# Optimization experiments

Measured on AMD Instinct MI355X. Metric: run time of the kernel, lower is better.

## Reference

```python
import jax, jax.numpy as jnp
import numpy as np

N = 4_194_304  # total points
C = 2          # classes: 0=ground, 1=plant
B = 8          # number of point clouds in the batch
SIGMA_L = 0.1
SIGMA_R = 0.4
CLAMP_FACTOR = 2.0
MIN_VAL = 0.1
FOCAL_GAMMA = 2.0
FOCAL_ALPHA = 1.0
LOSS_WEIGHT = 1.0


def setup_inputs() -> dict:
    key = jax.random.key(0)
    k1, k2, k3 = jax.random.split(key, 3)
    pred = jax.random.normal(k1, (N, C), dtype=jnp.float32)
    coord = jax.random.normal(k2, (N, 3), dtype=jnp.float32)
    segment = jax.random.randint(k3, (N,), 0, C, dtype=jnp.int32)
    # pointcept-style cumulative offsets: equal-sized clouds, offset[-1] == N
    offset = (jnp.arange(1, B + 1, dtype=jnp.int32) * (N // B))
    return {"pred": pred, "coord": coord, "segment": segment, "offset": offset}


def _gauss_weights(z, segment, batch):
    # per-cloud z_ground_max (fallback: z.min) and z_plant_min (fallback: z.max)
    neg_inf = jnp.array(-jnp.inf, z.dtype)
    pos_inf = jnp.array(jnp.inf, z.dtype)
    gmax = jax.ops.segment_max(jnp.where(segment == 0, z, neg_inf), batch, num_segments=B)
    pmin = jax.ops.segment_min(jnp.where(segment == 1, z, pos_inf), batch, num_segments=B)
    has_g = jax.ops.segment_sum((segment == 0).astype(z.dtype), batch, num_segments=B) > 0
    has_p = jax.ops.segment_sum((segment == 1).astype(z.dtype), batch, num_segments=B) > 0
    zmin = jax.ops.segment_min(z, batch, num_segments=B)
    zmax = jax.ops.segment_max(z, batch, num_segments=B)
    g = jnp.where(has_g, gmax, zmin)
    p = jnp.where(has_p, pmin, zmax)
    mu_b = g + (p - g) * 0.5  # (B,)
    mu = mu_b[batch]          # (N,)
    d = z - mu
    w_left = jnp.exp(-(d * d) / (2.0 * SIGMA_L * SIGMA_L))
    w_right = jnp.exp(-(d * d) / (2.0 * SIGMA_R * SIGMA_R))
    w_right = jnp.where(d > CLAMP_FACTOR * SIGMA_R, jnp.array(MIN_VAL, z.dtype), w_right)
    return jnp.where(z <= mu, w_left, w_right)


def reference(pred, coord, segment, offset):
    n = pred.shape[0]
    # offset2batch: per-point batch id from cumulative offsets
    batch = jnp.searchsorted(offset, jnp.arange(n, dtype=offset.dtype), side='right')
    # cross entropy (reduction='none')
    logp = jax.nn.log_softmax(pred, axis=1)              # (N, C)
    logp_t = jnp.take_along_axis(logp, segment[:, None], axis=1)[:, 0]  # (N,)
    seg_loss = (-logp_t) * LOSS_WEIGHT
    # focal reweighting (computed under no_grad in the original)
    p_t = jax.lax.stop_gradient(jnp.exp(logp_t))
    focal_weight = FOCAL_ALPHA * (1.0 - p_t) ** FOCAL_GAMMA
    seg_loss = seg_loss * focal_weight
    # asymmetric gaussian z-weighting, segment-conditioned per cloud
    weights = _gauss_weights(coord[:, 2], segment, batch)
    return jnp.mean(seg_loss * weights)
```

## Files before the change

### kernel.cpp

```cpp
#include <hip/hip_runtime.h>
#include <math.h>

#define THREADS 1024
#define NBLOCKS 256
#define UNROLL  8

__device__ __forceinline__ unsigned enc_f(float f) {
    unsigned b = __float_as_uint(f);
    return (b & 0x80000000u) ? ~b : (b | 0x80000000u);
}
__device__ __forceinline__ float dec_f(unsigned u) {
    unsigned b = (u & 0x80000000u) ? (u ^ 0x80000000u) : ~u;
    return __uint_as_float(b);
}
#define ENC_NEG_INF 0x007FFFFFu
#define ENC_POS_INF 0xFF800000u
__device__ __forceinline__ unsigned ident_w(int w) {
    return (w < 8 || w >= 24) ? ENC_NEG_INF : ENC_POS_INF;
}

#define SLOT(base, blk) ((base) + 64 + (blk) * 32)

#define CNT_B(ii, bdst) do { bdst = 0; \
    _Pragma("unroll") for (int j_ = 0; j_ < 8; ++j_) bdst += ((ii) >= roff[j_]); } while (0)

#define FLUSH_LDS(bb, g_, p_, mn_, mx_) do { \
    atomicMax(&s_stats[      (bb)], enc_f(g_));  \
    atomicMin(&s_stats[ 8  + (bb)], enc_f(p_));  \
    atomicMin(&s_stats[16  + (bb)], enc_f(mn_)); \
    atomicMax(&s_stats[24  + (bb)], enc_f(mx_)); } while (0)

__global__ __launch_bounds__(THREADS) void k_stats(
        const float* __restrict__ coord, const int* __restrict__ segment,
        const int* __restrict__ offset, unsigned* __restrict__ ws, int n, int nb) {
    __shared__ unsigned s_stats[32];
    const int tid = threadIdx.x;
    if (tid < 32) s_stats[tid] = ident_w(tid);
    if (blockIdx.x == 0 && tid == THREADS - 1) {
        *(double*)(ws + 32) = 0.0;
        ws[34] = 0u;
    }
    int roff[8];
    #pragma unroll
    for (int j = 0; j < 8; ++j) roff[j] = (j < nb) ? offset[j] : 0x7FFFFFFF;
    __syncthreads();

    const int chunk = (n + (int)gridDim.x - 1) / (int)gridDim.x;
    const int start = blockIdx.x * chunk;
    const int end   = min(n, start + chunk);

    float lg = -INFINITY, lp = INFINITY, lmn = INFINITY, lmx = -INFINITY;

    if (start < end) {
        int ba = 0, bb = 0;
        #pragma unroll
        for (int j = 0; j < 8; ++j) { ba += (start >= roff[j]); bb += ((end - 1) >= roff[j]); }
        if (ba == bb) {
            int i = start + tid;
            for (; i + (UNROLL - 1) * THREADS < end; i += UNROLL * THREADS) {
                float z[UNROLL]; int s[UNROLL];
                #pragma unroll
                for (int k = 0; k < UNROLL; ++k) z[k] = coord[3 * (i + k * THREADS) + 2];
                #pragma unroll
                for (int k = 0; k < UNROLL; ++k) s[k] = segment[i + k * THREADS];
                #pragma unroll
                for (int k = 0; k < UNROLL; ++k) {
                    lmn = fminf(lmn, z[k]);
                    lmx = fmaxf(lmx, z[k]);
                    lg  = fmaxf(lg, (s[k] == 0) ? z[k] : -INFINITY);
                    lp  = fminf(lp, (s[k] != 0) ? z[k] : INFINITY);
                }
            }
            for (; i < end; i += THREADS) {
                float z = coord[3 * i + 2]; int s = segment[i];
                lmn = fminf(lmn, z); lmx = fmaxf(lmx, z);
                lg  = fmaxf(lg, (s == 0) ? z : -INFINITY);
                lp  = fminf(lp, (s != 0) ? z : INFINITY);
            }
            #pragma unroll
            for (int m = 32; m; m >>= 1) {
                lg  = fmaxf(lg,  __shfl_xor(lg,  m, 64));
                lp  = fminf(lp,  __shfl_xor(lp,  m, 64));
                lmn = fminf(lmn, __shfl_xor(lmn, m, 64));
                lmx = fmaxf(lmx, __shfl_xor(lmx, m, 64));
            }
            if ((tid & 63) == 0) FLUSH_LDS(ba, lg, lp, lmn, lmx);
        } else {
            int curb = -1;
            for (int i = start + tid; i < end; i += THREADS) {
                float z = coord[3 * i + 2]; int s = segment[i], b;
                CNT_B(i, b);
                if (b != curb) {
                    if (curb >= 0) FLUSH_LDS(curb, lg, lp, lmn, lmx);
                    lg = -INFINITY; lp = INFINITY; lmn = INFINITY; lmx = -INFINITY;
                    curb = b;
                }
                lmn = fminf(lmn, z); lmx = fmaxf(lmx, z);
                if (s == 0) lg = fmaxf(lg, z); else lp = fminf(lp, z);
            }
            if (curb >= 0) FLUSH_LDS(curb, lg, lp, lmn, lmx);
        }
    }
    __syncthreads();
    if (tid < 32) SLOT(ws, blockIdx.x)[tid] = s_stats[tid];
}

__device__ __forceinline__ float point_loss(float p0, float p1, int s, float z, float mu) {
    float m   = fmaxf(p0, p1);
    float lse = m + logf(expf(p0 - m) + expf(p1 - m));
    float lpt = ((s == 0) ? p0 : p1) - lse;
    float pt  = expf(lpt);
    float om  = 1.0f - pt;
    float loss = -lpt * om * om;
    float d  = z - mu;
    float cf = (z <= mu) ? 50.0f : 3.125f;
    float w  = expf(-d * d * cf);
    if (z > mu && d > 0.8f) w = 0.1f;
    return loss * w;
}

__global__ __launch_bounds__(THREADS) void k_loss(
        const float* __restrict__ pred, const float* __restrict__ coord,
        const int* __restrict__ segment, const int* __restrict__ offset,
        unsigned* __restrict__ ws, float* __restrict__ out, int n, int nb) {
    __shared__ unsigned s_comb[32];
    __shared__ float    s_mu[8];
    __shared__ float    s_part[THREADS / 64];
    const int tid = threadIdx.x;
    int roff[8];
    #pragma unroll
    for (int j = 0; j < 8; ++j) roff[j] = (j < nb) ? offset[j] : 0x7FFFFFFF;

    if (tid < 32) s_comb[tid] = ident_w(tid);
    __syncthreads();
    {
        const int w = tid & 31, g = tid >> 5;
        unsigned v = ident_w(w);
        #pragma unroll
        for (int j = 0; j < NBLOCKS / 32; ++j) {
            unsigned u = SLOT((const unsigned*)ws, g * (NBLOCKS / 32) + j)[w];
            v = (w < 8 || w >= 24) ? max(v, u) : min(v, u);
        }
        if (w < 8 || w >= 24) atomicMax(&s_comb[w], v);
        else                  atomicMin(&s_comb[w], v);
    }
    __syncthreads();
    if (tid < 8) {
        unsigned ug = s_comb[tid], up = s_comb[8 + tid];
        float g = dec_f(ug), p = dec_f(up);
        if (ug == ENC_NEG_INF) g = dec_f(s_comb[16 + tid]);
        if (up == ENC_POS_INF) p = dec_f(s_comb[24 + tid]);
        s_mu[tid] = g + (p - g) * 0.5f;
    }
    __syncthreads();

    const int chunk = (n + (int)gridDim.x - 1) / (int)gridDim.x;
    const int start = blockIdx.x * chunk;
    const int end   = min(n, start + chunk);
    const float2* pred2 = (const float2*)pred;

    float lsum = 0.0f;
    if (start < end) {
        int ba = 0, bb = 0;
        #pragma unroll
        for (int j = 0; j < 8; ++j) { ba += (start >= roff[j]); bb += ((end - 1) >= roff[j]); }
        if (ba == bb) {
            const float mu = s_mu[ba];
            int i = start + tid;
            for (; i + (UNROLL - 1) * THREADS < end; i += UNROLL * THREADS) {
                float z[UNROLL]; int s[UNROLL]; float2 pp[UNROLL];
                #pragma unroll
                for (int k = 0; k < UNROLL; ++k) pp[k] = pred2[i + k * THREADS];
                #pragma unroll
                for (int k = 0; k < UNROLL; ++k) z[k] = coord[3 * (i + k * THREADS) + 2];
                #pragma unroll
                for (int k = 0; k < UNROLL; ++k) s[k] = segment[i + k * THREADS];
                #pragma unroll
                for (int k = 0; k < UNROLL; ++k)
                    lsum += point_loss(pp[k].x, pp[k].y, s[k], z[k], mu);
            }
            for (; i < end; i += THREADS) {
                float2 pp = pred2[i];
                lsum += point_loss(pp.x, pp.y, segment[i], coord[3 * i + 2], mu);
            }
        } else {
            for (int i = start + tid; i < end; i += THREADS) {
                int b; CNT_B(i, b);
                float2 pp = pred2[i];
                lsum += point_loss(pp.x, pp.y, segment[i], coord[3 * i + 2], s_mu[b]);
            }
        }
    }

    #pragma unroll
    for (int off = 32; off > 0; off >>= 1) lsum += __shfl_down(lsum, off, 64);
    if ((tid & 63) == 0) s_part[tid >> 6] = lsum;
    __syncthreads();
    if (tid == 0) {
        float t = 0.0f;
        #pragma unroll
        for (int wv = 0; wv < THREADS / 64; ++wv) t += s_part[wv];
        double* acc = (double*)(ws + 32);
        atomicAdd(acc, (double)t);
        __threadfence();
        unsigned c = atomicAdd(&ws[34], 1u);
        if (c == (unsigned)gridDim.x - 1u) {
            double v = atomicAdd(acc, 0.0);
            out[0] = (float)(v / (double)n);
        }
    }
}

extern "C" void kernel_launch(void* const* d_in, const int* in_sizes, int n_in,
                              void* d_out, int out_size, void* d_ws, size_t ws_size,
                              hipStream_t stream) {
    const float* pred    = (const float*)d_in[0];
    const float* coord   = (const float*)d_in[1];
    const int*   segment = (const int*)d_in[2];
    const int*   offset  = (const int*)d_in[3];
    const int n  = in_sizes[2];
    const int nb = in_sizes[3];

    unsigned* ws = (unsigned*)d_ws;

    hipLaunchKernelGGL(k_stats, dim3(NBLOCKS), dim3(THREADS), 0, stream,
                       coord, segment, offset, ws, n, nb);
    hipLaunchKernelGGL(k_loss,  dim3(NBLOCKS), dim3(THREADS), 0, stream,
                       pred, coord, segment, offset, ws, (float*)d_out, n, nb);
}
```

Before: 133.6 us.

## Simplify binary focal loss math, add nontemporal loads, deepen stats unroll

Rewrites the two-class cross-entropy and focal term using the logit difference, computing log1p(exp(-dlt)) and a hardware reciprocal instead of a max/log-sum-exp plus a second exp. All streaming loads in the stats and loss kernels become nontemporal, and the stats-kernel unroll goes from 8 to 16 to put more loads in flight. The aim is fewer transcendental instructions per point and less cache pollution on a bandwidth-bound pass. In exchange the hardware reciprocal and the clamp at 80 add small precision differences.

```diff
diff --git a/kernel.cpp b/kernel.cpp
--- a/kernel.cpp
+++ b/kernel.cpp
@@ -4,6 +4,9 @@
 #define THREADS 1024
 #define NBLOCKS 256
 #define UNROLL  8
+#define SUNROLL 16
+
+typedef __attribute__((ext_vector_type(2))) float f2v;
 
 __device__ __forceinline__ unsigned enc_f(float f) {
     unsigned b = __float_as_uint(f);
@@ -57,14 +60,16 @@
         for (int j = 0; j < 8; ++j) { ba += (start >= roff[j]); bb += ((end - 1) >= roff[j]); }
         if (ba == bb) {
             int i = start + tid;
-            for (; i + (UNROLL - 1) * THREADS < end; i += UNROLL * THREADS) {
-                float z[UNROLL]; int s[UNROLL];
-                #pragma unroll
-                for (int k = 0; k < UNROLL; ++k) z[k] = coord[3 * (i + k * THREADS) + 2];
-                #pragma unroll
-                for (int k = 0; k < UNROLL; ++k) s[k] = segment[i + k * THREADS];
-                #pragma unroll
-                for (int k = 0; k < UNROLL; ++k) {
+            for (; i + (SUNROLL - 1) * THREADS < end; i += SUNROLL * THREADS) {
+                float z[SUNROLL]; int s[SUNROLL];
+                #pragma unroll
+                for (int k = 0; k < SUNROLL; ++k)
+                    z[k] = __builtin_nontemporal_load(&coord[3 * (i + k * THREADS) + 2]);
+                #pragma unroll
+                for (int k = 0; k < SUNROLL; ++k)
+                    s[k] = __builtin_nontemporal_load(&segment[i + k * THREADS]);
+                #pragma unroll
+                for (int k = 0; k < SUNROLL; ++k) {
                     lmn = fminf(lmn, z[k]);
                     lmx = fmaxf(lmx, z[k]);
                     lg  = fmaxf(lg, (s[k] == 0) ? z[k] : -INFINITY);
@@ -106,16 +111,16 @@
 }
 
 __device__ __forceinline__ float point_loss(float p0, float p1, int s, float z, float mu) {
-    float m   = fmaxf(p0, p1);
-    float lse = m + logf(expf(p0 - m) + expf(p1 - m));
-    float lpt = ((s == 0) ? p0 : p1) - lse;
-    float pt  = expf(lpt);
-    float om  = 1.0f - pt;
-    float loss = -lpt * om * om;
+    float dlt = (s == 0) ? (p0 - p1) : (p1 - p0);
+    float u   = expf(fminf(-dlt, 80.0f));
+    float inv = __builtin_amdgcn_rcpf(1.0f + u);
+    float om  = u * inv;
+    float l1u = logf(1.0f + u);
+    float loss = l1u * om * om;
     float d  = z - mu;
     float cf = (z <= mu) ? 50.0f : 3.125f;
     float w  = expf(-d * d * cf);
-    if (z > mu && d > 0.8f) w = 0.1f;
+    if (d > 0.8f) w = 0.1f;
     return loss * w;
 }
 
@@ -157,7 +162,7 @@
     const int chunk = (n + (int)gridDim.x - 1) / (int)gridDim.x;
     const int start = blockIdx.x * chunk;
     const int end   = min(n, start + chunk);
-    const float2* pred2 = (const float2*)pred;
+    const f2v* pred2 = (const f2v*)pred;
 
     float lsum = 0.0f;
     if (start < end) {
@@ -168,25 +173,28 @@
             const float mu = s_mu[ba];
             int i = start + tid;
             for (; i + (UNROLL - 1) * THREADS < end; i += UNROLL * THREADS) {
-                float z[UNROLL]; int s[UNROLL]; float2 pp[UNROLL];
-                #pragma unroll
-                for (int k = 0; k < UNROLL; ++k) pp[k] = pred2[i + k * THREADS];
-                #pragma unroll
-                for (int k = 0; k < UNROLL; ++k) z[k] = coord[3 * (i + k * THREADS) + 2];
-                #pragma unroll
-                for (int k = 0; k < UNROLL; ++k) s[k] = segment[i + k * THREADS];
+                float z[UNROLL]; int s[UNROLL]; f2v pp[UNROLL];
+                #pragma unroll
+                for (int k = 0; k < UNROLL; ++k)
+                    pp[k] = __builtin_nontemporal_load(&pred2[i + k * THREADS]);
+                #pragma unroll
+                for (int k = 0; k < UNROLL; ++k)
+                    z[k] = __builtin_nontemporal_load(&coord[3 * (i + k * THREADS) + 2]);
+                #pragma unroll
+                for (int k = 0; k < UNROLL; ++k)
+                    s[k] = __builtin_nontemporal_load(&segment[i + k * THREADS]);
                 #pragma unroll
                 for (int k = 0; k < UNROLL; ++k)
                     lsum += point_loss(pp[k].x, pp[k].y, s[k], z[k], mu);
             }
             for (; i < end; i += THREADS) {
-                float2 pp = pred2[i];
+                f2v pp = pred2[i];
                 lsum += point_loss(pp.x, pp.y, segment[i], coord[3 * i + 2], mu);
             }
         } else {
             for (int i = start + tid; i < end; i += THREADS) {
                 int b; CNT_B(i, b);
-                float2 pp = pred2[i];
+                f2v pp = pred2[i];
                 lsum += point_loss(pp.x, pp.y, segment[i], coord[3 * i + 2], s_mu[b]);
             }
         }
```

New measurement: 137.2 us. +2.7%, slower.
